# Kernel optimization log

Hardware: AMD Instinct MI355X
Metric: run time of the kernel (lower is better)

Reference implementation:

```python
import jax, jax.numpy as jnp
import numpy as np

B = 1024           # number of jets (independent binary trees)
L = 10             # tree depth (levels); level j has B*2**j nodes
H = 128            # hidden size
FEAT = 7           # input features per node
LEVEL_SIZES = [B * 2**j for j in range(L)]
OFF = np.concatenate([[0], np.cumsum(LEVEL_SIZES)]).astype(int).tolist()
INNER = LEVEL_SIZES[:-1]                     # all non-bottom nodes are inner
COFF = np.concatenate([[0], np.cumsum(INNER)]).astype(int).tolist()


def _linear_init(key, fan_in, fan_out):
    return jax.random.normal(key, (fan_in, fan_out), jnp.float32) / np.sqrt(fan_in).astype(np.float32)


def setup_inputs() -> dict:
    key = jax.random.key(0)
    ks = jax.random.split(key, 6)
    contents = jax.random.normal(ks[0], (OFF[-1], FEAT), jnp.float32)
    # child indices are local to level j+1: node k at level j -> children (2k, 2k+1)
    ch = [np.stack([2 * np.arange(n), 2 * np.arange(n) + 1], axis=1) for n in INNER]
    children = jnp.asarray(np.concatenate(ch, axis=0), jnp.int32)
    return {
        "contents": contents,
        "children": children,
        "W_u": _linear_init(ks[1], FEAT, H), "b_u": jnp.zeros((H,), jnp.float32),
        "W_h": _linear_init(ks[2], 3 * H, H), "b_h": jnp.zeros((H,), jnp.float32),
        "W_z": _linear_init(ks[3], 4 * H, 4 * H), "b_z": jnp.zeros((4 * H,), jnp.float32),
        "W_r": _linear_init(ks[4], 3 * H, 3 * H), "b_r": jnp.zeros((3 * H,), jnp.float32),
        "conv_w": jnp.asarray([0.9], jnp.float32),
        "conv_b": jnp.asarray([0.01], jnp.float32),
    }


def reference(contents, children, W_u, b_u, W_h, b_h, W_z, b_z, W_r, b_r, conv_w, conv_b):
    def conv_chain(x):
        # relu(conv1x1(relu(conv1x1(relu(conv1x1(x)))))): Conv2d(1,1,1) == scalar scale + bias
        for _ in range(3):
            x = jax.nn.relu(conv_w[0] * x + conv_b[0])
        return x

    emb = None  # embeddings of the level below (level j+1)
    for j in reversed(range(L)):
        c = contents[OFF[j]:OFF[j + 1]]               # [N_j, FEAT]
        u = conv_chain(c @ W_u + b_u)                 # [N_j, H]
        if j == L - 1:                                # bottom level: all leaves
            emb = u
            continue
        ch = children[COFF[j]:COFF[j + 1]]            # [N_j, 2] indices into level j+1
        h_L = emb[ch[:, 0]]                           # gather left children
        h_R = emb[ch[:, 1]]                           # gather right children
        hhu = jnp.concatenate([h_L, h_R, u], axis=1)  # [N_j, 3H]
        r = jax.nn.sigmoid(hhu @ W_r + b_r)           # reset gate
        h_H = conv_chain((r * hhu) @ W_h + b_h)       # [N_j, H]
        z = jnp.concatenate([h_H, hhu], axis=1) @ W_z + b_z  # [N_j, 4H]
        g = jax.nn.softmax(
            jnp.stack([z[:, :H], z[:, H:2 * H], z[:, 2 * H:3 * H], z[:, 3 * H:]], axis=-1),
            axis=-1,
        )                                             # [N_j, H, 4] gate weights
        emb = g[..., 0] * h_H + g[..., 1] * h_L + g[..., 2] * h_R + g[..., 3] * u
    return emb.reshape(B, -1)                         # [B, H] root embeddings
```

## Files before the change

### kernel.cpp

```cpp
#include <hip/hip_runtime.h>
#include <hip/hip_bf16.h>

typedef _Float16 f16x8 __attribute__((ext_vector_type(8)));
typedef _Float16 f16x4 __attribute__((ext_vector_type(4)));
typedef float f32x4 __attribute__((ext_vector_type(4)));

#define H 128
#define FEAT 7
#define RB 64
#define NT 512

__device__ __forceinline__ float conv3(float x, float w, float b) {
    x = fmaxf(fmaf(w, x, b), 0.f);
    x = fmaxf(fmaf(w, x, b), 0.f);
    x = fmaxf(fmaf(w, x, b), 0.f);
    return x;
}
__device__ __forceinline__ float sigm(float x) {
    return __builtin_amdgcn_rcpf(1.f + __expf(-x));
}

__global__ __launch_bounds__(256) void pack_weights(
    const float* __restrict__ Wr, const float* __restrict__ Wh, const float* __restrict__ Wz,
    _Float16* __restrict__ Pr, _Float16* __restrict__ Ph, _Float16* __restrict__ Pz)
{
    int idx = blockIdx.x * 256 + threadIdx.x;
    if (idx < 384 * 384) {
        int k = idx / 384, n = idx % 384;
        Pr[((size_t)(k >> 3) * 384 + n) * 8 + (k & 7)] = (_Float16)Wr[idx];
    }
    if (idx < 384 * 128) {
        int k = idx / 128, n = idx % 128;
        Ph[((size_t)(k >> 3) * 128 + n) * 8 + (k & 7)] = (_Float16)Wh[idx];
    }
    if (idx < 512 * 512) {
        int k = idx / 512, n = idx % 512;
        Pz[((size_t)(k >> 3) * 512 + n) * 8 + (k & 7)] = (_Float16)Wz[idx];
    }
}

template<bool LEAF>
__global__ __launch_bounds__(NT, 2) void level_kernel(
    const float* __restrict__ contents,
    const int* __restrict__ children,
    const float* __restrict__ leafContents,
    const _Float16* __restrict__ embPrev,
    _Float16* __restrict__ embOut,
    float* __restrict__ finalOut,
    const float* __restrict__ Wu, const float* __restrict__ bu,
    const _Float16* __restrict__ Pr, const float* __restrict__ br,
    const _Float16* __restrict__ Ph, const float* __restrict__ bh,
    const _Float16* __restrict__ Pz, const float* __restrict__ bz,
    const float* __restrict__ convw, const float* __restrict__ convb)
{
    __shared__ __align__(16) _Float16 s_hhu[RB][392];
    __shared__ __align__(16) _Float16 s_x[RB][392];
    _Float16 (* const s_hH)[136] = (_Float16 (*)[136])&s_x[0][0];

    const int t = threadIdx.x;
    const int row0 = blockIdx.x * RB;
    const int col0 = t & 127;
    const int tq = t >> 7;
    const float cw = convw[0], cbv = convb[0];

    const int lane = t & 63;
    const int w = t >> 6;
    const int q = lane >> 4;
    const int ln = lane & 15;

    const f16x8* PBc = (const f16x8*)Pr + (w * 48 + ln);
    f16x8 awc[3][3];
#pragma unroll
    for (int c = 0; c < 3; c++) awc[0][c] = PBc[(size_t)q * 384 + c * 16];
#pragma unroll
    for (int c = 0; c < 3; c++) awc[1][c] = PBc[(size_t)(4 + q) * 384 + c * 16];

    float wcol[FEAT];
#pragma unroll
    for (int k = 0; k < FEAT; k++) wcol[k] = Wu[k * H + col0];
    const float bucol = bu[col0];

#pragma unroll 4
    for (int i = 0; i < 16; i++) {
        int r = i * 4 + tq;
        const float* c = contents + (size_t)(row0 + r) * FEAT;
        float acc = bucol;
#pragma unroll
        for (int k = 0; k < FEAT; k++) acc = fmaf(c[k], wcol[k], acc);
        s_hhu[r][256 + col0] = (_Float16)conv3(acc, cw, cbv);
    }

    if (LEAF) {
#pragma unroll 4
        for (int i = 0; i < 32; i++) {
            int cr = i * 4 + tq;
            int child = children[row0 * 2 + cr];
            const float* c = leafContents + (size_t)child * FEAT;
            float acc = bucol;
#pragma unroll
            for (int k = 0; k < FEAT; k++) acc = fmaf(c[k], wcol[k], acc);
            s_hhu[cr >> 1][(cr & 1) * 128 + col0] = (_Float16)conv3(acc, cw, cbv);
        }
    } else {
        int rp = t >> 4, chunk = t & 15;
#pragma unroll
        for (int p = 0; p < 4; p++) {
            int cr = p * 32 + rp;
            int child = children[row0 * 2 + cr];
            uint4 v = *(const uint4*)(embPrev + (size_t)child * H + chunk * 8);
            *(uint4*)&s_hhu[cr >> 1][(cr & 1) * 128 + chunk * 8] = v;
        }
    }
    __syncthreads();

    const f16x8* PBd = (const f16x8*)Ph + (w * 16 + ln);
    f16x8 awd[3];

    {
        f32x4 acc[3][4];
#pragma unroll
        for (int c = 0; c < 3; c++)
#pragma unroll
            for (int rt = 0; rt < 4; rt++) acc[c][rt] = (f32x4){0,0,0,0};
        f16x8 b[4];
#pragma unroll
        for (int rt = 0; rt < 4; rt++) b[rt] = *(const f16x8*)&s_hhu[rt * 16 + ln][q * 8];
#pragma unroll
        for (int kk = 0; kk < 12; kk++) {
            if (kk + 2 < 12) {
                int kb = (kk + 2) * 4 + q;
#pragma unroll
                for (int c = 0; c < 3; c++) awc[(kk + 2) % 3][c] = PBc[(size_t)kb * 384 + c * 16];
            }
            f16x8 cb[4];
#pragma unroll
            for (int rt = 0; rt < 4; rt++) cb[rt] = b[rt];
            if (kk < 11) {
#pragma unroll
                for (int rt = 0; rt < 4; rt++)
                    b[rt] = *(const f16x8*)&s_hhu[rt * 16 + ln][(kk + 1) * 32 + q * 8];
            }
#pragma unroll
            for (int c = 0; c < 3; c++)
#pragma unroll
                for (int rt = 0; rt < 4; rt++)
                    acc[c][rt] = __builtin_amdgcn_mfma_f32_16x16x32_f16(awc[kk % 3][c], cb[rt], acc[c][rt], 0, 0, 0);
        }
        awd[0] = PBd[(size_t)q * 128];
        awd[1] = PBd[(size_t)(4 + q) * 128];
#pragma unroll
        for (int c = 0; c < 3; c++) {
            int fb = w * 48 + c * 16 + q * 4;
            f32x4 bv = *(const f32x4*)&br[fb];
#pragma unroll
            for (int rt = 0; rt < 4; rt++) {
                int row = rt * 16 + ln;
                f16x4 hh = *(const f16x4*)&s_hhu[row][fb];
                f16x4 xv;
#pragma unroll
                for (int reg = 0; reg < 4; reg++) {
                    float rv = sigm(acc[c][rt][reg] + bv[reg]);
                    xv[reg] = (_Float16)(rv * (float)hh[reg]);
                }
                *(f16x4*)&s_x[row][fb] = xv;
            }
        }
    }
    __syncthreads();

    const f16x8* PBe = (const f16x8*)Pz + (w * 16 + ln);
    f16x8 awe[3][4];

    {
        f32x4 acc[4];
#pragma unroll
        for (int rt = 0; rt < 4; rt++) acc[rt] = (f32x4){0,0,0,0};
        f16x8 b[4];
#pragma unroll
        for (int rt = 0; rt < 4; rt++) b[rt] = *(const f16x8*)&s_x[rt * 16 + ln][q * 8];
#pragma unroll
        for (int kk = 0; kk < 12; kk++) {
            if (kk + 2 < 12) {
                int kb = (kk + 2) * 4 + q;
                awd[(kk + 2) % 3] = PBd[(size_t)kb * 128];
            }
            f16x8 cb[4];
#pragma unroll
            for (int rt = 0; rt < 4; rt++) cb[rt] = b[rt];
            if (kk < 11) {
#pragma unroll
                for (int rt = 0; rt < 4; rt++)
                    b[rt] = *(const f16x8*)&s_x[rt * 16 + ln][(kk + 1) * 32 + q * 8];
            }
#pragma unroll
            for (int rt = 0; rt < 4; rt++)
                acc[rt] = __builtin_amdgcn_mfma_f32_16x16x32_f16(awd[kk % 3], cb[rt], acc[rt], 0, 0, 0);
        }
#pragma unroll
        for (int g = 0; g < 4; g++) awe[0][g] = PBe[(size_t)q * 512 + g * 128];
#pragma unroll
        for (int g = 0; g < 4; g++) awe[1][g] = PBe[(size_t)(4 + q) * 512 + g * 128];
        float hv[4][4];
        int fb = w * 16 + q * 4;
        f32x4 bhv = *(const f32x4*)&bh[fb];
#pragma unroll
        for (int rt = 0; rt < 4; rt++)
#pragma unroll
            for (int reg = 0; reg < 4; reg++)
                hv[rt][reg] = conv3(acc[rt][reg] + bhv[reg], cw, cbv);
        __syncthreads();
#pragma unroll
        for (int rt = 0; rt < 4; rt++) {
            f16x4 hp;
#pragma unroll
            for (int reg = 0; reg < 4; reg++) hp[reg] = (_Float16)hv[rt][reg];
            *(f16x4*)&s_hH[rt * 16 + ln][fb] = hp;
        }
    }
    __syncthreads();

    {
        const int nb = w * 16;
        f32x4 acc[4][4];
#pragma unroll
        for (int g = 0; g < 4; g++)
#pragma unroll
            for (int rt = 0; rt < 4; rt++) acc[g][rt] = (f32x4){0,0,0,0};
        f16x8 b[4];
#pragma unroll
        for (int rt = 0; rt < 4; rt++) b[rt] = *(const f16x8*)&s_hH[rt * 16 + ln][q * 8];
#pragma unroll
        for (int kk = 0; kk < 16; kk++) {
            if (kk + 2 < 16) {
                int kb = (kk + 2) * 4 + q;
#pragma unroll
                for (int g = 0; g < 4; g++) awe[(kk + 2) % 3][g] = PBe[(size_t)kb * 512 + g * 128];
            }
            f16x8 cb[4];
#pragma unroll
            for (int rt = 0; rt < 4; rt++) cb[rt] = b[rt];
            if (kk < 15) {
                if (kk + 1 < 4) {
#pragma unroll
                    for (int rt = 0; rt < 4; rt++)
                        b[rt] = *(const f16x8*)&s_hH[rt * 16 + ln][(kk + 1) * 32 + q * 8];
                } else {
                    int k0 = (kk + 1) * 32 - 128;
#pragma unroll
                    for (int rt = 0; rt < 4; rt++)
                        b[rt] = *(const f16x8*)&s_hhu[rt * 16 + ln][k0 + q * 8];
                }
            }
#pragma unroll
            for (int g = 0; g < 4; g++)
#pragma unroll
                for (int rt = 0; rt < 4; rt++)
                    acc[g][rt] = __builtin_amdgcn_mfma_f32_16x16x32_f16(awe[kk % 3][g], cb[rt], acc[g][rt], 0, 0, 0);
        }
        int colb = nb + q * 4;
        f32x4 bz0 = *(const f32x4*)&bz[colb];
        f32x4 bz1 = *(const f32x4*)&bz[128 + colb];
        f32x4 bz2 = *(const f32x4*)&bz[256 + colb];
        f32x4 bz3 = *(const f32x4*)&bz[384 + colb];
#pragma unroll
        for (int rt = 0; rt < 4; rt++) {
            int row = rt * 16 + ln;
            f16x4 hH4 = *(const f16x4*)&s_hH[row][colb];
            f16x4 hL4 = *(const f16x4*)&s_hhu[row][colb];
            f16x4 hR4 = *(const f16x4*)&s_hhu[row][128 + colb];
            f16x4 u4  = *(const f16x4*)&s_hhu[row][256 + colb];
            size_t gidx = (size_t)(row0 + row) * H + colb;
            if (finalOut) {
                f32x4 ov;
#pragma unroll
                for (int reg = 0; reg < 4; reg++) {
                    float z0 = acc[0][rt][reg] + bz0[reg];
                    float z1 = acc[1][rt][reg] + bz1[reg];
                    float z2 = acc[2][rt][reg] + bz2[reg];
                    float z3 = acc[3][rt][reg] + bz3[reg];
                    float m = fmaxf(fmaxf(z0, z1), fmaxf(z2, z3));
                    float e0 = __expf(z0 - m), e1 = __expf(z1 - m), e2 = __expf(z2 - m), e3 = __expf(z3 - m);
                    float inv = __builtin_amdgcn_rcpf(e0 + e1 + e2 + e3);
                    ov[reg] = (e0 * (float)hH4[reg] + e1 * (float)hL4[reg] +
                               e2 * (float)hR4[reg] + e3 * (float)u4[reg]) * inv;
                }
                *(f32x4*)&finalOut[gidx] = ov;
            } else {
                f16x4 ev;
#pragma unroll
                for (int reg = 0; reg < 4; reg++) {
                    float z0 = acc[0][rt][reg] + bz0[reg];
                    float z1 = acc[1][rt][reg] + bz1[reg];
                    float z2 = acc[2][rt][reg] + bz2[reg];
                    float z3 = acc[3][rt][reg] + bz3[reg];
                    float m = fmaxf(fmaxf(z0, z1), fmaxf(z2, z3));
                    float e0 = __expf(z0 - m), e1 = __expf(z1 - m), e2 = __expf(z2 - m), e3 = __expf(z3 - m);
                    float inv = __builtin_amdgcn_rcpf(e0 + e1 + e2 + e3);
                    ev[reg] = (_Float16)((e0 * (float)hH4[reg] + e1 * (float)hL4[reg] +
                                          e2 * (float)hR4[reg] + e3 * (float)u4[reg]) * inv);
                }
                *(f16x4*)&embOut[gidx] = ev;
            }
        }
    }
}

extern "C" void kernel_launch(void* const* d_in, const int* in_sizes, int n_in,
                              void* d_out, int out_size, void* d_ws, size_t ws_size,
                              hipStream_t stream) {
    const float* contents = (const float*)d_in[0];
    const int*   children = (const int*)d_in[1];
    const float* Wu = (const float*)d_in[2];
    const float* bu = (const float*)d_in[3];
    const float* Wh = (const float*)d_in[4];
    const float* bh = (const float*)d_in[5];
    const float* Wz = (const float*)d_in[6];
    const float* bz = (const float*)d_in[7];
    const float* Wr = (const float*)d_in[8];
    const float* br = (const float*)d_in[9];
    const float* convw = (const float*)d_in[10];
    const float* convb = (const float*)d_in[11];
    float* out = (float*)d_out;

    _Float16* Pr = (_Float16*)d_ws;
    _Float16* Ph = Pr + 384 * 384;
    _Float16* Pz = Ph + 384 * 128;
    _Float16* bufA = (_Float16*)((char*)d_ws + (1 << 20));
    _Float16* bufB = bufA + (size_t)262144 * H;

    auto OFFS = [](int j) -> long long { return 1024LL * ((1LL << j) - 1); };

    pack_weights<<<(512 * 512 + 255) / 256, 256, 0, stream>>>(Wr, Wh, Wz, Pr, Ph, Pz);

    {
        int n = 1024 << 8;
        level_kernel<true><<<n / RB, NT, 0, stream>>>(
            contents + OFFS(8) * FEAT, children + OFFS(8) * 2,
            contents + OFFS(9) * FEAT, nullptr, bufA, nullptr,
            Wu, bu, Pr, br, Ph, bh, Pz, bz, convw, convb);
    }

    _Float16* prev = bufA;
    _Float16* cur  = bufB;
    for (int j = 7; j >= 0; j--) {
        int n = 1024 << j;
        level_kernel<false><<<n / RB, NT, 0, stream>>>(
            contents + OFFS(j) * FEAT, children + OFFS(j) * 2,
            nullptr, prev, cur, (j == 0 ? out : nullptr),
            Wu, bu, Pr, br, Ph, bh, Pz, bz, convw, convb);
        _Float16* tmp = prev; prev = cur; cur = tmp;
    }
}
```

Baseline: 798.4 us.

## Give h_H its own LDS buffer and triple-buffer shared-memory B operands

Moves s_hH out of the s_x alias into a dedicated shared array, which removes the barrier that previously separated the final reads of s_x from the h_H writes. All three MFMA GEMM loops now prefetch the LDS B fragments two k-steps ahead into a three-slot register ring, matching the existing weight prefetch depth. This adds about 17KB of LDS per block and extra VGPRs, which could lower occupancy below the two blocks per CU requested by launch bounds.

```diff
diff --git a/kernel.cpp b/kernel.cpp
--- a/kernel.cpp
+++ b/kernel.cpp
@@ -55,7 +55,7 @@
 {
     __shared__ __align__(16) _Float16 s_hhu[RB][392];
     __shared__ __align__(16) _Float16 s_x[RB][392];
-    _Float16 (* const s_hH)[136] = (_Float16 (*)[136])&s_x[0][0];
+    __shared__ __align__(16) _Float16 s_hH[RB][136];
 
     const int t = threadIdx.x;
     const int row0 = blockIdx.x * RB;
@@ -122,29 +122,26 @@
         for (int c = 0; c < 3; c++)
 #pragma unroll
             for (int rt = 0; rt < 4; rt++) acc[c][rt] = (f32x4){0,0,0,0};
-        f16x8 b[4];
-#pragma unroll
-        for (int rt = 0; rt < 4; rt++) b[rt] = *(const f16x8*)&s_hhu[rt * 16 + ln][q * 8];
+        f16x8 bb[3][4];
+#pragma unroll
+        for (int rt = 0; rt < 4; rt++) bb[0][rt] = *(const f16x8*)&s_hhu[rt * 16 + ln][q * 8];
+#pragma unroll
+        for (int rt = 0; rt < 4; rt++) bb[1][rt] = *(const f16x8*)&s_hhu[rt * 16 + ln][32 + q * 8];
 #pragma unroll
         for (int kk = 0; kk < 12; kk++) {
             if (kk + 2 < 12) {
                 int kb = (kk + 2) * 4 + q;
 #pragma unroll
                 for (int c = 0; c < 3; c++) awc[(kk + 2) % 3][c] = PBc[(size_t)kb * 384 + c * 16];
-            }
-            f16x8 cb[4];
-#pragma unroll
-            for (int rt = 0; rt < 4; rt++) cb[rt] = b[rt];
-            if (kk < 11) {
 #pragma unroll
                 for (int rt = 0; rt < 4; rt++)
-                    b[rt] = *(const f16x8*)&s_hhu[rt * 16 + ln][(kk + 1) * 32 + q * 8];
+                    bb[(kk + 2) % 3][rt] = *(const f16x8*)&s_hhu[rt * 16 + ln][(kk + 2) * 32 + q * 8];
             }
 #pragma unroll
             for (int c = 0; c < 3; c++)
 #pragma unroll
                 for (int rt = 0; rt < 4; rt++)
-                    acc[c][rt] = __builtin_amdgcn_mfma_f32_16x16x32_f16(awc[kk % 3][c], cb[rt], acc[c][rt], 0, 0, 0);
+                    acc[c][rt] = __builtin_amdgcn_mfma_f32_16x16x32_f16(awc[kk % 3][c], bb[kk % 3][rt], acc[c][rt], 0, 0, 0);
         }
         awd[0] = PBd[(size_t)q * 128];
         awd[1] = PBd[(size_t)(4 + q) * 128];
@@ -175,45 +172,36 @@
         f32x4 acc[4];
 #pragma unroll
         for (int rt = 0; rt < 4; rt++) acc[rt] = (f32x4){0,0,0,0};
-        f16x8 b[4];
-#pragma unroll
-        for (int rt = 0; rt < 4; rt++) b[rt] = *(const f16x8*)&s_x[rt * 16 + ln][q * 8];
+        f16x8 bb[3][4];
+#pragma unroll
+        for (int rt = 0; rt < 4; rt++) bb[0][rt] = *(const f16x8*)&s_x[rt * 16 + ln][q * 8];
+#pragma unroll
+        for (int rt = 0; rt < 4; rt++) bb[1][rt] = *(const f16x8*)&s_x[rt * 16 + ln][32 + q * 8];
 #pragma unroll
         for (int kk = 0; kk < 12; kk++) {
             if (kk + 2 < 12) {
                 int kb = (kk + 2) * 4 + q;
                 awd[(kk + 2) % 3] = PBd[(size_t)kb * 128];
-            }
-            f16x8 cb[4];
-#pragma unroll
-            for (int rt = 0; rt < 4; rt++) cb[rt] = b[rt];
-            if (kk < 11) {
 #pragma unroll
                 for (int rt = 0; rt < 4; rt++)
-                    b[rt] = *(const f16x8*)&s_x[rt * 16 + ln][(kk + 1) * 32 + q * 8];
+                    bb[(kk + 2) % 3][rt] = *(const f16x8*)&s_x[rt * 16 + ln][(kk + 2) * 32 + q * 8];
             }
 #pragma unroll
             for (int rt = 0; rt < 4; rt++)
-                acc[rt] = __builtin_amdgcn_mfma_f32_16x16x32_f16(awd[kk % 3], cb[rt], acc[rt], 0, 0, 0);
+                acc[rt] = __builtin_amdgcn_mfma_f32_16x16x32_f16(awd[kk % 3], bb[kk % 3][rt], acc[rt], 0, 0, 0);
         }
 #pragma unroll
         for (int g = 0; g < 4; g++) awe[0][g] = PBe[(size_t)q * 512 + g * 128];
 #pragma unroll
         for (int g = 0; g < 4; g++) awe[1][g] = PBe[(size_t)(4 + q) * 512 + g * 128];
-        float hv[4][4];
         int fb = w * 16 + q * 4;
         f32x4 bhv = *(const f32x4*)&bh[fb];
 #pragma unroll
-        for (int rt = 0; rt < 4; rt++)
-#pragma unroll
-            for (int reg = 0; reg < 4; reg++)
-                hv[rt][reg] = conv3(acc[rt][reg] + bhv[reg], cw, cbv);
-        __syncthreads();
-#pragma unroll
         for (int rt = 0; rt < 4; rt++) {
             f16x4 hp;
 #pragma unroll
-            for (int reg = 0; reg < 4; reg++) hp[reg] = (_Float16)hv[rt][reg];
+            for (int reg = 0; reg < 4; reg++)
+                hp[reg] = (_Float16)conv3(acc[rt][reg] + bhv[reg], cw, cbv);
             *(f16x4*)&s_hH[rt * 16 + ln][fb] = hp;
         }
     }
@@ -226,36 +214,33 @@
         for (int g = 0; g < 4; g++)
 #pragma unroll
             for (int rt = 0; rt < 4; rt++) acc[g][rt] = (f32x4){0,0,0,0};
-        f16x8 b[4];
-#pragma unroll
-        for (int rt = 0; rt < 4; rt++) b[rt] = *(const f16x8*)&s_hH[rt * 16 + ln][q * 8];
+        f16x8 bb[3][4];
+#pragma unroll
+        for (int rt = 0; rt < 4; rt++) bb[0][rt] = *(const f16x8*)&s_hH[rt * 16 + ln][q * 8];
+#pragma unroll
+        for (int rt = 0; rt < 4; rt++) bb[1][rt] = *(const f16x8*)&s_hH[rt * 16 + ln][32 + q * 8];
 #pragma unroll
         for (int kk = 0; kk < 16; kk++) {
             if (kk + 2 < 16) {
                 int kb = (kk + 2) * 4 + q;
 #pragma unroll
                 for (int g = 0; g < 4; g++) awe[(kk + 2) % 3][g] = PBe[(size_t)kb * 512 + g * 128];
-            }
-            f16x8 cb[4];
-#pragma unroll
-            for (int rt = 0; rt < 4; rt++) cb[rt] = b[rt];
-            if (kk < 15) {
-                if (kk + 1 < 4) {
+                if (kk + 2 < 4) {
 #pragma unroll
                     for (int rt = 0; rt < 4; rt++)
-                        b[rt] = *(const f16x8*)&s_hH[rt * 16 + ln][(kk + 1) * 32 + q * 8];
+                        bb[(kk + 2) % 3][rt] = *(const f16x8*)&s_hH[rt * 16 + ln][(kk + 2) * 32 + q * 8];
                 } else {
-                    int k0 = (kk + 1) * 32 - 128;
+                    int k0 = (kk + 2) * 32 - 128;
 #pragma unroll
                     for (int rt = 0; rt < 4; rt++)
-                        b[rt] = *(const f16x8*)&s_hhu[rt * 16 + ln][k0 + q * 8];
+                        bb[(kk + 2) % 3][rt] = *(const f16x8*)&s_hhu[rt * 16 + ln][k0 + q * 8];
                 }
             }
 #pragma unroll
             for (int g = 0; g < 4; g++)
 #pragma unroll
                 for (int rt = 0; rt < 4; rt++)
-                    acc[g][rt] = __builtin_amdgcn_mfma_f32_16x16x32_f16(awe[kk % 3][g], cb[rt], acc[g][rt], 0, 0, 0);
+                    acc[g][rt] = __builtin_amdgcn_mfma_f32_16x16x32_f16(awe[kk % 3][g], bb[kk % 3][rt], acc[g][rt], 0, 0, 0);
         }
         int colb = nb + q * 4;
         f32x4 bz0 = *(const f32x4*)&bz[colb];
```

Measured after the change: 786.4 us. No clear change (-1.5%).
